# Performance work log

Measured on AMD Instinct MI355X. Metric: run time of the kernel, lower is better.

## Reference

```python
import jax, jax.numpy as jnp
import numpy as np
import math

B, S, L, H, NH, FF, V = 32, 512, 12, 768, 12, 3072, 30522
DH = H // NH


def setup_inputs() -> dict:
    key = jax.random.key(0)
    ks = jax.random.split(key, 16)
    w = lambda k, shape: (jax.random.normal(k, shape, jnp.float32) * 0.02)
    return {
        "input_ids": jax.random.randint(ks[0], (B, S), 0, V, dtype=jnp.int32),
        "attention_mask": jax.random.uniform(ks[1], (B, S), jnp.float32),
        "word_emb": w(ks[2], (V, H)),
        "pos_emb": w(ks[3], (S, H)),
        "type_emb": w(ks[4], (H,)),
        "ln_emb_s": jnp.ones((H,), jnp.float32),
        "ln_emb_b": jnp.zeros((H,), jnp.float32),
        "Wq": w(ks[5], (L, H, H)), "bq": jnp.zeros((L, H), jnp.float32),
        "Wk": w(ks[6], (L, H, H)), "bk": jnp.zeros((L, H), jnp.float32),
        "Wv": w(ks[7], (L, H, H)), "bv": jnp.zeros((L, H), jnp.float32),
        "Wo": w(ks[8], (L, H, H)), "bo": jnp.zeros((L, H), jnp.float32),
        "ln1_s": jnp.ones((L, H), jnp.float32), "ln1_b": jnp.zeros((L, H), jnp.float32),
        "Wi": w(ks[9], (L, H, FF)), "bi": jnp.zeros((L, FF), jnp.float32),
        "Wf": w(ks[10], (L, FF, H)), "bf": jnp.zeros((L, H), jnp.float32),
        "ln2_s": jnp.ones((L, H), jnp.float32), "ln2_b": jnp.zeros((L, H), jnp.float32),
    }


def _ln(x, s, b):
    # BERT LayerNorm, eps=1e-12
    m = jnp.mean(x, -1, keepdims=True)
    v = jnp.mean((x - m) ** 2, -1, keepdims=True)
    return (x - m) * jax.lax.rsqrt(v + 1e-12) * s + b


def reference(input_ids, attention_mask, word_emb, pos_emb, type_emb,
              ln_emb_s, ln_emb_b, Wq, bq, Wk, bk, Wv, bv, Wo, bo,
              ln1_s, ln1_b, Wi, bi, Wf, bf, ln2_s, ln2_b):
    b, s = input_ids.shape
    scale = 1.0 / math.sqrt(DH)
    # Embeddings: word + position + (single) token-type, then LayerNorm
    h = word_emb[input_ids] + pos_emb[None, :s] + type_emb
    h = _ln(h, ln_emb_s, ln_emb_b)
    key_mask = attention_mask[:, None, None, :]  # [B,1,1,S], float

    def layer(h, p):
        wq, bq_, wk, bk_, wv, bv_, wo, bo_, l1s, l1b, wi, bi_, wf, bf_, l2s, l2b = p
        q = (jnp.einsum('bsd,de->bse', h, wq) + bq_).reshape(b, s, NH, DH)
        k = (jnp.einsum('bsd,de->bse', h, wk) + bk_).reshape(b, s, NH, DH)
        v = (jnp.einsum('bsd,de->bse', h, wv) + bv_).reshape(b, s, NH, DH)
        scores = jnp.einsum('bqhd,bkhd->bhqk', q, k) * scale
        probs = jax.nn.softmax(scores, axis=-1)
        # post-softmax masking + renormalization (the non-standard part)
        probs = probs * key_mask
        probs = probs / jnp.clip(jnp.sum(probs, -1, keepdims=True), 1e-9, None)
        ctx = jnp.einsum('bhqk,bkhd->bqhd', probs, v).reshape(b, s, H)
        attn_out = _ln(jnp.einsum('bsd,de->bse', ctx, wo) + bo_ + h, l1s, l1b)
        inter = jax.nn.gelu(jnp.einsum('bsd,df->bsf', attn_out, wi) + bi_, approximate=False)
        out = _ln(jnp.einsum('bsf,fd->bsd', inter, wf) + bf_ + attn_out, l2s, l2b)
        return out, None

    h, _ = jax.lax.scan(layer, h, (Wq, bq, Wk, bk, Wv, bv, Wo, bo,
                                   ln1_s, ln1_b, Wi, bi, Wf, bf, ln2_s, ln2_b))
    # masked mean pooling + L2 normalize (normalize=True)
    m = attention_mask[..., None]
    sent = jnp.sum(h * m, axis=1) / jnp.clip(jnp.sum(m, axis=1), 1e-6, None)
    sent = sent / jnp.clip(jnp.linalg.norm(sent, axis=-1, keepdims=True), 1e-12, None)
    return sent
```

## Files before the change

kernel.cpp:

```cpp
#include <hip/hip_runtime.h>
#include <hip/hip_bf16.h>
#include <math.h>

typedef __bf16 bf16;
typedef __bf16 bf16x8 __attribute__((ext_vector_type(8)));
typedef float  f32x4  __attribute__((ext_vector_type(4)));

#define B_  32
#define S_  512
#define H_  768
#define NH_ 12
#define DH_ 64
#define FF_ 3072
#define L_  12
#define M_  (B_*S_)
#define QKV_ 2304

#define VST 516
#define PST 68

__device__ __forceinline__ void gload16(const bf16* g, bf16* l) {
  __builtin_amdgcn_global_load_lds(
      (const __attribute__((address_space(1))) void*)g,
      (__attribute__((address_space(3))) void*)l, 16, 0, 0);
}

__device__ __forceinline__ float fast_gelu(float x) {
  float z = x * 0.70710678118f;
  float s = fabsf(z);
  float t = __builtin_amdgcn_rcpf(1.0f + 0.3275911f * s);
  float p = t*(0.254829592f + t*(-0.284496736f + t*(1.421413741f +
            t*(-1.453152027f + t*1.061405429f))));
  float e = p * __expf(-s*s);
  float erfv = copysignf(1.0f - e, z);
  return 0.5f * x * (1.0f + erfv);
}

__global__ __launch_bounds__(512, 4) void gemm128(
    const bf16* __restrict__ A, const bf16* __restrict__ Bt,
    const float* __restrict__ bias, void* __restrict__ outp,
    int N, int K, int tiles_n, int epi)
{
  __shared__ bf16 As[128*64];
  __shared__ bf16 Bs[128*64];
  const int tid  = threadIdx.x;
  const int lane = tid & 63, wid = tid >> 6;
  const int wr = wid >> 2, wc = wid & 3;
  const int lrow = lane & 15, kgrp = lane >> 4;

  const int nwg = gridDim.x, orig = blockIdx.x;
  const int qc = nwg >> 3, rc = nwg & 7;
  const int xcd = orig & 7, lin = orig >> 3;
  const int wg = (xcd < rc ? xcd*(qc+1) : rc*(qc+1) + (xcd-rc)*qc) + lin;
  const int tm = wg / tiles_n, tn = wg % tiles_n;
  const size_t m0 = (size_t)tm * 128, n0 = (size_t)tn * 128;
  const int KT = K >> 6;

  const bf16* Ab = A  + m0 * K;
  const bf16* Bb = Bt + n0 * K;

  auto stage = [&](const bf16* gbase, bf16* ldsbase, int kt) {
#pragma unroll
    for (int j = 0; j < 2; ++j) {
      int lin2  = j*512 + tid;
      int prow  = lin2 >> 3;
      int pslot = lin2 & 7;
      int lslot = pslot ^ (prow & 7);
      const bf16* src = gbase + (size_t)prow * K + (size_t)kt*64 + lslot*8;
      bf16* dst = ldsbase + (size_t)(j*512 + (wid<<6))*8;
      gload16(src, dst);
    }
  };

  f32x4 acc[4][2] = {};

  for (int t = 0; t < KT; ++t) {
    __syncthreads();
    stage(Ab, As, t);
    stage(Bb, Bs, t);
    __syncthreads();
#pragma unroll
    for (int kk = 0; kk < 2; ++kk) {
      bf16x8 a[4], b[2];
#pragma unroll
      for (int m = 0; m < 4; ++m) {
        int row  = wr*64 + m*16 + lrow;
        int slot = (kk*4 + kgrp) ^ (lrow & 7);
        a[m] = *(const bf16x8*)&As[row*64 + slot*8];
      }
#pragma unroll
      for (int n = 0; n < 2; ++n) {
        int row  = wc*32 + n*16 + lrow;
        int slot = (kk*4 + kgrp) ^ (lrow & 7);
        b[n] = *(const bf16x8*)&Bs[row*64 + slot*8];
      }
#pragma unroll
      for (int m = 0; m < 4; ++m)
#pragma unroll
        for (int n = 0; n < 2; ++n)
          acc[m][n] = __builtin_amdgcn_mfma_f32_16x16x32_bf16(a[m], b[n], acc[m][n], 0, 0, 0);
    }
  }

#pragma unroll
  for (int m = 0; m < 4; ++m)
#pragma unroll
    for (int n = 0; n < 2; ++n) {
      int col = (int)n0 + wc*32 + n*16 + lrow;
      float bv = bias[col];
#pragma unroll
      for (int r = 0; r < 4; ++r) {
        int row = (int)m0 + wr*64 + m*16 + kgrp*4 + r;
        float x = acc[m][n][r] + bv;
        size_t idx = (size_t)row * N + col;
        if (epi == 1)      ((float*)outp)[idx] = x;
        else if (epi == 0) ((bf16*)outp)[idx]  = (bf16)x;
        else               ((bf16*)outp)[idx]  = (bf16)fast_gelu(x);
      }
    }
}

__global__ __launch_bounds__(256) void weight_prep(
    const float* __restrict__ Wq, const float* __restrict__ Wk,
    const float* __restrict__ Wv, const float* __restrict__ Wo,
    const float* __restrict__ Wi, const float* __restrict__ Wf,
    const float* __restrict__ bq, const float* __restrict__ bk,
    const float* __restrict__ bv,
    bf16* __restrict__ wqkv, bf16* __restrict__ wot,
    bf16* __restrict__ wit,  bf16* __restrict__ wft,
    float* __restrict__ qkbias)
{
  int bid = blockIdx.x;
  if (bid >= 1728) {
    int i = (bid - 1728)*256 + threadIdx.x;
    if (i < QKV_)
      qkbias[i] = (i < 768) ? bq[i] : (i < 1536 ? bk[i-768] : bv[i-1536]);
    return;
  }
  const float* W; bf16* Wt; int K, N, t;
  if (bid < 576) {
    K = 768; N = 768;
    if      (bid < 144) { W = Wq; Wt = wqkv;             t = bid; }
    else if (bid < 288) { W = Wk; Wt = wqkv + 768*768;   t = bid - 144; }
    else if (bid < 432) { W = Wv; Wt = wqkv + 2*768*768; t = bid - 288; }
    else                { W = Wo; Wt = wot;              t = bid - 432; }
  } else if (bid < 1152) { W = Wi; Wt = wit; K = 768;  N = 3072; t = bid - 576; }
  else                   { W = Wf; Wt = wft; K = 3072; N = 768;  t = bid - 1152; }
  const int kt = K >> 6;
  const int k0 = (t % kt)*64, n0 = (t / kt)*64;

  __shared__ bf16 T[64][65];
  int tx = threadIdx.x & 63, ty = threadIdx.x >> 6;
#pragma unroll
  for (int j = 0; j < 16; ++j) {
    int kk = j*4 + ty;
    T[kk][tx] = (bf16)W[(size_t)(k0+kk)*N + n0 + tx];
  }
  __syncthreads();
#pragma unroll
  for (int j = 0; j < 16; ++j) {
    int nn = j*4 + ty;
    Wt[(size_t)(n0+nn)*K + k0 + tx] = T[tx][nn];
  }
}

__device__ __forceinline__ void block_sum2(float& a, float& b, float* red) {
  int lane = threadIdx.x & 63, wid = threadIdx.x >> 6;
  for (int o = 32; o > 0; o >>= 1) { a += __shfl_xor(a, o); b += __shfl_xor(b, o); }
  if (lane == 0) { red[wid*2] = a; red[wid*2+1] = b; }
  __syncthreads();
  a = red[0] + red[2] + red[4] + red[6];
  b = red[1] + red[3] + red[5] + red[7];
  __syncthreads();
}

__global__ __launch_bounds__(256) void embed_ln(
    const int* __restrict__ ids, const float* __restrict__ we,
    const float* __restrict__ pe, const float* __restrict__ te,
    const float* __restrict__ gs, const float* __restrict__ gb,
    float* __restrict__ h32, bf16* __restrict__ hb)
{
  __shared__ float red[8];
  int row = blockIdx.x;
  int s = row & (S_-1);
  int id = ids[row];
  int t = threadIdx.x;
  float x[3], sum = 0.f, sq = 0.f;
#pragma unroll
  for (int j = 0; j < 3; ++j) {
    int c = t + j*256;
    float v = we[(size_t)id*H_ + c] + pe[(size_t)s*H_ + c] + te[c];
    x[j] = v; sum += v; sq += v*v;
  }
  block_sum2(sum, sq, red);
  float mean = sum * (1.f/H_);
  float var  = sq  * (1.f/H_) - mean*mean;
  float rstd = rsqrtf(fmaxf(var, 0.f) + 1e-12f);
#pragma unroll
  for (int j = 0; j < 3; ++j) {
    int c = t + j*256;
    float y = (x[j]-mean)*rstd*gs[c] + gb[c];
    h32[(size_t)row*H_ + c] = y;
    hb [(size_t)row*H_ + c] = (bf16)y;
  }
}

__global__ __launch_bounds__(256) void ln_res(
    const float* __restrict__ t32, const float* __restrict__ res,
    const float* __restrict__ gs, const float* __restrict__ gb,
    float* __restrict__ o32, bf16* __restrict__ ob)
{
  __shared__ float red[8];
  int row = blockIdx.x, t = threadIdx.x;
  float x[3], sum = 0.f, sq = 0.f;
#pragma unroll
  for (int j = 0; j < 3; ++j) {
    int c = t + j*256;
    float v = t32[(size_t)row*H_ + c] + res[(size_t)row*H_ + c];
    x[j] = v; sum += v; sq += v*v;
  }
  block_sum2(sum, sq, red);
  float mean = sum * (1.f/H_);
  float var  = sq  * (1.f/H_) - mean*mean;
  float rstd = rsqrtf(fmaxf(var, 0.f) + 1e-12f);
#pragma unroll
  for (int j = 0; j < 3; ++j) {
    int c = t + j*256;
    float y = (x[j]-mean)*rstd*gs[c] + gb[c];
    o32[(size_t)row*H_ + c] = y;
    ob [(size_t)row*H_ + c] = (bf16)y;
  }
}

__global__ __launch_bounds__(512, 2) void attn_kernel(
    const bf16* __restrict__ qkv, const float* __restrict__ mask,
    bf16* __restrict__ ctx)
{
  __shared__ bf16 Kl[S_*64];
  __shared__ bf16 Vt[DH_*VST];
  __shared__ float mk[S_];
  __shared__ bf16 Pl[8][16*PST];
  int tid = threadIdx.x, lane = tid & 63, wid = tid >> 6;
  int lrow = lane & 15, kgrp = lane >> 4;
  int cur_head = -1;

  for (int u = 0; u < 6; ++u) {
    int unit = blockIdx.x*6 + u;
    int hh = unit >> 2, pass = unit & 3;
    int b = hh / NH_, h = hh % NH_;
    const bf16* Qb = qkv + (size_t)(b*S_)*QKV_ + h*DH_;

    if (hh != cur_head) {
      __syncthreads();
      const bf16* Kb = qkv + (size_t)(b*S_)*QKV_ + H_   + h*DH_;
      const bf16* Vb = qkv + (size_t)(b*S_)*QKV_ + 2*H_ + h*DH_;
#pragma unroll
      for (int it = 0; it < 8; ++it) {
        int lin   = it*512 + tid;
        int prow  = lin >> 3;
        int pslot = lin & 7;
        int lslot = pslot ^ (prow & 7);
        gload16(&Kb[(size_t)prow*QKV_ + lslot*8],
                &Kl[(size_t)(it*512 + (wid<<6))*8]);
      }
      for (int it = 0; it < 8; ++it) {
        int slot = it*512 + tid;
        int s = slot >> 3, c8 = (slot & 7)*8;
        bf16x8 v = *(const bf16x8*)&Vb[(size_t)s*QKV_ + c8];
#pragma unroll
        for (int i = 0; i < 8; ++i) Vt[(c8+i)*VST + s] = v[i];
      }
      mk[tid] = mask[b*S_ + tid];
      cur_head = hh;
      __syncthreads();
    }

    int q0 = pass*128 + wid*16;
    bf16x8 qa[2];
#pragma unroll
    for (int kc = 0; kc < 2; ++kc) {
      qa[kc] = *(const bf16x8*)&Qb[(size_t)(q0 + lrow)*QKV_ + kc*32 + kgrp*8];
#pragma unroll
      for (int i = 0; i < 8; ++i)
        qa[kc][i] = (bf16)((float)qa[kc][i] * 0.125f);
    }
    f32x4 O[4] = {};
    float mrun[4], lrun[4];
#pragma unroll
    for (int r = 0; r < 4; ++r) { mrun[r] = -1e30f; lrun[r] = 0.f; }

    for (int c0 = 0; c0 < S_; c0 += 64) {
      f32x4 Sf[4] = {};
      __builtin_amdgcn_s_setprio(1);
#pragma unroll
      for (int kc = 0; kc < 2; ++kc)
#pragma unroll
        for (int sn = 0; sn < 4; ++sn) {
          int row  = c0 + sn*16 + lrow;
          int slot = (kc*4 + kgrp) ^ (lrow & 7);
          bf16x8 kbv = *(const bf16x8*)&Kl[(size_t)row*64 + slot*8];
          Sf[sn] = __builtin_amdgcn_mfma_f32_16x16x32_bf16(qa[kc], kbv, Sf[sn], 0, 0, 0);
        }
      __builtin_amdgcn_s_setprio(0);
      float cmax[4];
#pragma unroll
      for (int r = 0; r < 4; ++r) cmax[r] = -1e30f;
#pragma unroll
      for (int sn = 0; sn < 4; ++sn)
#pragma unroll
        for (int r = 0; r < 4; ++r)
          cmax[r] = fmaxf(cmax[r], Sf[sn][r]);
      for (int o = 1; o < 16; o <<= 1)
#pragma unroll
        for (int r = 0; r < 4; ++r) cmax[r] = fmaxf(cmax[r], __shfl_xor(cmax[r], o));

      bool small = (cmax[0] <= mrun[0]+8.f) && (cmax[1] <= mrun[1]+8.f) &&
                   (cmax[2] <= mrun[2]+8.f) && (cmax[3] <= mrun[3]+8.f);
      bool skip = __all(small);
      float newm[4], fr[4], lsum[4];
      if (skip) {
#pragma unroll
        for (int r = 0; r < 4; ++r) { newm[r] = mrun[r]; fr[r] = 1.f; lsum[r] = 0.f; }
      } else {
#pragma unroll
        for (int r = 0; r < 4; ++r) {
          newm[r] = fmaxf(mrun[r], cmax[r]);
          fr[r]   = __expf(mrun[r] - newm[r]);
          lsum[r] = 0.f;
        }
      }
#pragma unroll
      for (int sn = 0; sn < 4; ++sn) {
        float mkv = mk[c0 + sn*16 + lrow];
#pragma unroll
        for (int r = 0; r < 4; ++r) {
          float e = __expf(Sf[sn][r] - newm[r]) * mkv;
          bf16 eb = (bf16)e;
          lsum[r] += (float)eb;
          Pl[wid][(kgrp*4 + r)*PST + sn*16 + lrow] = eb;
        }
      }
      if (!skip) {
#pragma unroll
        for (int on = 0; on < 4; ++on)
#pragma unroll
          for (int r = 0; r < 4; ++r) O[on][r] *= fr[r];
      }
      asm volatile("s_waitcnt lgkmcnt(0)" ::: "memory");
      __builtin_amdgcn_sched_barrier(0);
      __builtin_amdgcn_s_setprio(1);
#pragma unroll
      for (int kc = 0; kc < 2; ++kc) {
        bf16x8 pa = *(const bf16x8*)&Pl[wid][lrow*PST + kc*32 + kgrp*8];
#pragma unroll
        for (int on = 0; on < 4; ++on) {
          bf16x8 vv = *(const bf16x8*)&Vt[(on*16 + lrow)*VST + c0 + kc*32 + kgrp*8];
          O[on] = __builtin_amdgcn_mfma_f32_16x16x32_bf16(pa, vv, O[on], 0, 0, 0);
        }
      }
      __builtin_amdgcn_s_setprio(0);
      for (int o = 1; o < 16; o <<= 1)
#pragma unroll
        for (int r = 0; r < 4; ++r) lsum[r] += __shfl_xor(lsum[r], o);
#pragma unroll
      for (int r = 0; r < 4; ++r) { lrun[r] = lrun[r]*fr[r] + lsum[r]; mrun[r] = newm[r]; }
    }
#pragma unroll
    for (int on = 0; on < 4; ++on)
#pragma unroll
      for (int r = 0; r < 4; ++r) {
        float val = O[on][r] / fmaxf(lrun[r], 1e-9f);
        int q = q0 + kgrp*4 + r;
        ctx[(size_t)(b*S_ + q)*H_ + h*DH_ + on*16 + lrow] = (bf16)val;
      }
  }
}

__global__ __launch_bounds__(256) void pool_partial(
    const float* __restrict__ h32, const float* __restrict__ mask,
    float* __restrict__ part)
{
  int b = blockIdx.x >> 3, ch = blockIdx.x & 7;
  int t = threadIdx.x;
  float a0 = 0.f, a1 = 0.f, a2 = 0.f;
  for (int s = ch*64; s < ch*64 + 64; ++s) {
    float m = mask[b*S_ + s];
    const float* hp = &h32[((size_t)b*S_ + s)*H_];
    a0 += hp[t]*m; a1 += hp[t+256]*m; a2 += hp[t+512]*m;
  }
  float* pp = &part[(size_t)(b*8 + ch)*H_];
  pp[t] = a0; pp[t+256] = a1; pp[t+512] = a2;
}

__global__ __launch_bounds__(256) void pool_final(
    const float* __restrict__ part, const float* __restrict__ mask,
    float* __restrict__ out)
{
  __shared__ float red[8];
  int b = blockIdx.x, t = threadIdx.x;
  float s0 = 0.f, s1 = 0.f, s2 = 0.f;
#pragma unroll
  for (int ch = 0; ch < 8; ++ch) {
    const float* pp = &part[(size_t)(b*8 + ch)*H_];
    s0 += pp[t]; s1 += pp[t+256]; s2 += pp[t+512];
  }
  float msum = mask[b*S_ + t] + mask[b*S_ + 256 + t];
  float dummy = 0.f;
  block_sum2(msum, dummy, red);
  float inv = 1.f / fmaxf(msum, 1e-6f);
  s0 *= inv; s1 *= inv; s2 *= inv;
  float nrm = s0*s0 + s1*s1 + s2*s2;
  dummy = 0.f;
  block_sum2(nrm, dummy, red);
  float rn = 1.f / fmaxf(sqrtf(nrm), 1e-12f);
  out[b*H_ + t]       = s0*rn;
  out[b*H_ + t + 256] = s1*rn;
  out[b*H_ + t + 512] = s2*rn;
}

extern "C" void kernel_launch(void* const* d_in, const int* in_sizes, int n_in,
                              void* d_out, int out_size, void* d_ws, size_t ws_size,
                              hipStream_t stream)
{
  const int*   ids  = (const int*)  d_in[0];
  const float* mask = (const float*)d_in[1];
  const float* we   = (const float*)d_in[2];
  const float* pe   = (const float*)d_in[3];
  const float* te   = (const float*)d_in[4];
  const float* les  = (const float*)d_in[5];
  const float* leb  = (const float*)d_in[6];
  const float* Wq   = (const float*)d_in[7];
  const float* bq   = (const float*)d_in[8];
  const float* Wk   = (const float*)d_in[9];
  const float* bk   = (const float*)d_in[10];
  const float* Wv   = (const float*)d_in[11];
  const float* bv   = (const float*)d_in[12];
  const float* Wo   = (const float*)d_in[13];
  const float* bo   = (const float*)d_in[14];
  const float* l1s  = (const float*)d_in[15];
  const float* l1b  = (const float*)d_in[16];
  const float* Wi   = (const float*)d_in[17];
  const float* bi   = (const float*)d_in[18];
  const float* Wf   = (const float*)d_in[19];
  const float* bfp  = (const float*)d_in[20];
  const float* l2s  = (const float*)d_in[21];
  const float* l2b  = (const float*)d_in[22];

  char* p = (char*)d_ws;
  auto alloc = [&](size_t bytes) { char* q = p; p += (bytes + 255) & ~(size_t)255; return q; };
  bf16*  wqkv = (bf16*) alloc((size_t)QKV_*H_*2);
  bf16*  wot  = (bf16*) alloc((size_t)H_*H_*2);
  bf16*  wit  = (bf16*) alloc((size_t)H_*FF_*2);
  bf16*  wft  = (bf16*) alloc((size_t)H_*FF_*2);
  float* qkbias=(float*)alloc((size_t)QKV_*4);
  bf16*  hb   = (bf16*) alloc((size_t)M_*H_*2);
  float* h32  = (float*)alloc((size_t)M_*H_*4);
  float* a32  = (float*)alloc((size_t)M_*H_*4);
  float* tmp  = (float*)alloc((size_t)M_*H_*4);
  bf16*  qkvb = (bf16*) alloc((size_t)M_*QKV_*2);
  bf16*  cxb  = (bf16*) alloc((size_t)M_*H_*2);
  bf16*  inb  = (bf16*) alloc((size_t)M_*FF_*2);
  float* part = (float*)alloc((size_t)B_*8*H_*4);

  embed_ln<<<M_, 256, 0, stream>>>(ids, we, pe, te, les, leb, h32, hb);

  for (int l = 0; l < L_; ++l) {
    size_t wsq = (size_t)l*H_*H_;
    weight_prep<<<1737, 256, 0, stream>>>(
        Wq + wsq, Wk + wsq, Wv + wsq, Wo + wsq,
        Wi + (size_t)l*H_*FF_, Wf + (size_t)l*FF_*H_,
        bq + l*H_, bk + l*H_, bv + l*H_,
        wqkv, wot, wit, wft, qkbias);

    gemm128<<<128*(QKV_/128), 512, 0, stream>>>(hb,  wqkv, qkbias,      qkvb, QKV_, H_,  QKV_/128, 0);
    attn_kernel<<<256, 512, 0, stream>>>(qkvb, mask, cxb);
    gemm128<<<128*(H_/128),  512, 0, stream>>>(cxb, wot, bo  + l*H_,  tmp,  H_,  H_,  H_/128,  1);
    ln_res<<<M_, 256, 0, stream>>>(tmp, h32, l1s + l*H_, l1b + l*H_, a32, hb);
    gemm128<<<128*(FF_/128), 512, 0, stream>>>(hb,  wit, bi  + l*FF_, inb,  FF_, H_,  FF_/128, 2);
    gemm128<<<128*(H_/128),  512, 0, stream>>>(inb, wft, bfp + l*H_,  tmp,  H_,  FF_, H_/128,  1);
    ln_res<<<M_, 256, 0, stream>>>(tmp, a32, l2s + l*H_, l2b + l*H_, h32, hb);
  }

  pool_partial<<<B_*8, 256, 0, stream>>>(h32, mask, part);
  pool_final<<<B_, 256, 0, stream>>>(part, mask, (float*)d_out);
}
```

Before: 5.383 ms.

## Store GEMM outputs as bf16 and compute softmax row sums via MFMA

The Wo and FFN-down GEMMs now write bf16 instead of fp32 into a temporary buffer, and the residual LayerNorm reads bf16. This halves the write and read traffic of those intermediates at some cost in precision. The attention kernel also drops its per-chunk cross-lane max and sum shuffles on the skip path. It computes the softmax denominator with an extra MFMA against a ones vector, and only reduces the max across lanes when a rescale is needed.

```diff
diff --git a/kernel.cpp b/kernel.cpp
--- a/kernel.cpp
+++ b/kernel.cpp
@@ -206,7 +206,7 @@
 }
 
 __global__ __launch_bounds__(256) void ln_res(
-    const float* __restrict__ t32, const float* __restrict__ res,
+    const bf16* __restrict__ t16, const float* __restrict__ res,
     const float* __restrict__ gs, const float* __restrict__ gb,
     float* __restrict__ o32, bf16* __restrict__ ob)
 {
@@ -216,7 +216,7 @@
 #pragma unroll
   for (int j = 0; j < 3; ++j) {
     int c = t + j*256;
-    float v = t32[(size_t)row*H_ + c] + res[(size_t)row*H_ + c];
+    float v = (float)t16[(size_t)row*H_ + c] + res[(size_t)row*H_ + c];
     x[j] = v; sum += v; sq += v*v;
   }
   block_sum2(sum, sq, red);
@@ -244,6 +244,10 @@
   int lrow = lane & 15, kgrp = lane >> 4;
   int cur_head = -1;
 
+  bf16x8 onesv;
+#pragma unroll
+  for (int i = 0; i < 8; ++i) onesv[i] = (bf16)1.0f;
+
   for (int u = 0; u < 6; ++u) {
     int unit = blockIdx.x*6 + u;
     int hh = unit >> 2, pass = unit & 3;
@@ -285,9 +289,10 @@
         qa[kc][i] = (bf16)((float)qa[kc][i] * 0.125f);
     }
     f32x4 O[4] = {};
-    float mrun[4], lrun[4];
-#pragma unroll
-    for (int r = 0; r < 4; ++r) { mrun[r] = -1e30f; lrun[r] = 0.f; }
+    f32x4 O5 = {};
+    float mrun[4];
+#pragma unroll
+    for (int r = 0; r < 4; ++r) mrun[r] = -1e30f;
 
     for (int c0 = 0; c0 < S_; c0 += 64) {
       f32x4 Sf[4] = {};
@@ -302,31 +307,33 @@
           Sf[sn] = __builtin_amdgcn_mfma_f32_16x16x32_bf16(qa[kc], kbv, Sf[sn], 0, 0, 0);
         }
       __builtin_amdgcn_s_setprio(0);
-      float cmax[4];
-#pragma unroll
-      for (int r = 0; r < 4; ++r) cmax[r] = -1e30f;
-#pragma unroll
-      for (int sn = 0; sn < 4; ++sn)
-#pragma unroll
-        for (int r = 0; r < 4; ++r)
-          cmax[r] = fmaxf(cmax[r], Sf[sn][r]);
-      for (int o = 1; o < 16; o <<= 1)
-#pragma unroll
-        for (int r = 0; r < 4; ++r) cmax[r] = fmaxf(cmax[r], __shfl_xor(cmax[r], o));
-
-      bool small = (cmax[0] <= mrun[0]+8.f) && (cmax[1] <= mrun[1]+8.f) &&
-                   (cmax[2] <= mrun[2]+8.f) && (cmax[3] <= mrun[3]+8.f);
+
+      float lm[4];
+#pragma unroll
+      for (int r = 0; r < 4; ++r)
+        lm[r] = fmaxf(fmaxf(Sf[0][r], Sf[1][r]), fmaxf(Sf[2][r], Sf[3][r]));
+      bool small = (lm[0] <= mrun[0]+8.f) && (lm[1] <= mrun[1]+8.f) &&
+                   (lm[2] <= mrun[2]+8.f) && (lm[3] <= mrun[3]+8.f);
       bool skip = __all(small);
-      float newm[4], fr[4], lsum[4];
+      float newm[4];
       if (skip) {
 #pragma unroll
-        for (int r = 0; r < 4; ++r) { newm[r] = mrun[r]; fr[r] = 1.f; lsum[r] = 0.f; }
+        for (int r = 0; r < 4; ++r) newm[r] = mrun[r];
       } else {
+        float cmax[4];
+#pragma unroll
+        for (int r = 0; r < 4; ++r) cmax[r] = lm[r];
+        for (int o = 1; o < 16; o <<= 1)
+#pragma unroll
+          for (int r = 0; r < 4; ++r) cmax[r] = fmaxf(cmax[r], __shfl_xor(cmax[r], o));
 #pragma unroll
         for (int r = 0; r < 4; ++r) {
           newm[r] = fmaxf(mrun[r], cmax[r]);
-          fr[r]   = __expf(mrun[r] - newm[r]);
-          lsum[r] = 0.f;
+          float fr = __expf(mrun[r] - newm[r]);
+#pragma unroll
+          for (int on = 0; on < 4; ++on) O[on][r] *= fr;
+          O5[r] *= fr;
+          mrun[r] = newm[r];
         }
       }
 #pragma unroll
@@ -335,16 +342,8 @@
 #pragma unroll
         for (int r = 0; r < 4; ++r) {
           float e = __expf(Sf[sn][r] - newm[r]) * mkv;
-          bf16 eb = (bf16)e;
-          lsum[r] += (float)eb;
-          Pl[wid][(kgrp*4 + r)*PST + sn*16 + lrow] = eb;
+          Pl[wid][(kgrp*4 + r)*PST + sn*16 + lrow] = (bf16)e;
         }
-      }
-      if (!skip) {
-#pragma unroll
-        for (int on = 0; on < 4; ++on)
-#pragma unroll
-          for (int r = 0; r < 4; ++r) O[on][r] *= fr[r];
       }
       asm volatile("s_waitcnt lgkmcnt(0)" ::: "memory");
       __builtin_amdgcn_sched_barrier(0);
@@ -357,19 +356,15 @@
           bf16x8 vv = *(const bf16x8*)&Vt[(on*16 + lrow)*VST + c0 + kc*32 + kgrp*8];
           O[on] = __builtin_amdgcn_mfma_f32_16x16x32_bf16(pa, vv, O[on], 0, 0, 0);
         }
+        O5 = __builtin_amdgcn_mfma_f32_16x16x32_bf16(pa, onesv, O5, 0, 0, 0);
       }
       __builtin_amdgcn_s_setprio(0);
-      for (int o = 1; o < 16; o <<= 1)
-#pragma unroll
-        for (int r = 0; r < 4; ++r) lsum[r] += __shfl_xor(lsum[r], o);
-#pragma unroll
-      for (int r = 0; r < 4; ++r) { lrun[r] = lrun[r]*fr[r] + lsum[r]; mrun[r] = newm[r]; }
     }
 #pragma unroll
     for (int on = 0; on < 4; ++on)
 #pragma unroll
       for (int r = 0; r < 4; ++r) {
-        float val = O[on][r] / fmaxf(lrun[r], 1e-9f);
+        float val = O[on][r] / fmaxf(O5[r], 1e-9f);
         int q = q0 + kgrp*4 + r;
         ctx[(size_t)(b*S_ + q)*H_ + h*DH_ + on*16 + lrow] = (bf16)val;
       }
@@ -456,7 +451,7 @@
   bf16*  hb   = (bf16*) alloc((size_t)M_*H_*2);
   float* h32  = (float*)alloc((size_t)M_*H_*4);
   float* a32  = (float*)alloc((size_t)M_*H_*4);
-  float* tmp  = (float*)alloc((size_t)M_*H_*4);
+  bf16*  tmpb = (bf16*) alloc((size_t)M_*H_*2);
   bf16*  qkvb = (bf16*) alloc((size_t)M_*QKV_*2);
   bf16*  cxb  = (bf16*) alloc((size_t)M_*H_*2);
   bf16*  inb  = (bf16*) alloc((size_t)M_*FF_*2);
@@ -474,11 +469,11 @@
 
     gemm128<<<128*(QKV_/128), 512, 0, stream>>>(hb,  wqkv, qkbias,      qkvb, QKV_, H_,  QKV_/128, 0);
     attn_kernel<<<256, 512, 0, stream>>>(qkvb, mask, cxb);
-    gemm128<<<128*(H_/128),  512, 0, stream>>>(cxb, wot, bo  + l*H_,  tmp,  H_,  H_,  H_/128,  1);
-    ln_res<<<M_, 256, 0, stream>>>(tmp, h32, l1s + l*H_, l1b + l*H_, a32, hb);
+    gemm128<<<128*(H_/128),  512, 0, stream>>>(cxb, wot, bo  + l*H_,  tmpb, H_,  H_,  H_/128,  0);
+    ln_res<<<M_, 256, 0, stream>>>(tmpb, h32, l1s + l*H_, l1b + l*H_, a32, hb);
     gemm128<<<128*(FF_/128), 512, 0, stream>>>(hb,  wit, bi  + l*FF_, inb,  FF_, H_,  FF_/128, 2);
-    gemm128<<<128*(H_/128),  512, 0, stream>>>(inb, wft, bfp + l*H_,  tmp,  H_,  FF_, H_/128,  1);
-    ln_res<<<M_, 256, 0, stream>>>(tmp, a32, l2s + l*H_, l2b + l*H_, h32, hb);
+    gemm128<<<128*(H_/128),  512, 0, stream>>>(inb, wft, bfp + l*H_,  tmpb, H_,  FF_, H_/128,  0);
+    ln_res<<<M_, 256, 0, stream>>>(tmpb, a32, l2s + l*H_, l2b + l*H_, h32, hb);
   }
 
   pool_partial<<<B_*8, 256, 0, stream>>>(h32, mask, part);
```

Measured after the change: 4.964 ms. 7.8% less time.
